# Optimization experiments

Measured on AMD Instinct MI355X. Metric: run time of the kernel, lower is better.

Reference implementation:

```python
import jax, jax.numpy as jnp
import numpy as np

DIM = 1024


def setup_inputs() -> dict:
    key = jax.random.key(0)
    ks = jax.random.split(key, 10)
    B, S, D = 4, 2048, DIM
    std = 1.0 / np.sqrt(D)  # torch Linear default uniform bound
    return {
        "query": jax.random.normal(ks[0], (B, S, D), jnp.float32),
        "key": jax.random.normal(ks[1], (B, S, D), jnp.float32),
        "value": jax.random.normal(ks[2], (B, S, D), jnp.float32),
        "context": jnp.zeros((D,), jnp.float32),
        "Wq": jax.random.uniform(ks[3], (D, D), jnp.float32, -std, std),
        "bq": jax.random.uniform(ks[4], (D,), jnp.float32, -std, std),
        "Wk": jax.random.uniform(ks[5], (D, D), jnp.float32, -std, std),
        "bk": jax.random.uniform(ks[6], (D,), jnp.float32, -std, std),
        "Wv": jax.random.uniform(ks[7], (D, D), jnp.float32, -std, std),
        "bv": jax.random.uniform(ks[8], (D,), jnp.float32, -std, std),
    }


def reference(query, key, value, context, Wq, bq, Wk, bk, Wv, bv):
    scale = query.shape[-1] ** -0.5
    # torch Linear: x @ W.T + b
    q = (query + context) @ Wq.T + bq          # [B,S,D]
    k = (key + context) @ Wk.T + bk            # [B,S,D]
    v = value @ Wv.T + bv                      # [B,S,D]
    scores = jnp.einsum("bqd,bkd->bqk", q, k) * scale  # [B,S,S]
    weights = jax.nn.softmax(scores, axis=-1)
    return jnp.einsum("bqk,bkd->bqd", weights, v)
```

## Files before the change

### kernel.cpp

```cpp
#include <hip/hip_runtime.h>

typedef __attribute__((ext_vector_type(8))) short bf16x8;
typedef __attribute__((ext_vector_type(4))) float floatx4;

constexpr int BATCH = 4;
constexpr int SEQ   = 2048;
constexpr int DIMN  = 1024;
constexpr int M1    = BATCH * SEQ;

__device__ __forceinline__ short f2bf(float f) {
    union { float f; unsigned u; } x; x.f = f;
    unsigned r = x.u + 0x7fffu + ((x.u >> 16) & 1u);
    return (short)(r >> 16);
}
__device__ __forceinline__ float bf2f(short s) {
    union { unsigned u; float f; } x; x.u = ((unsigned)(unsigned short)s) << 16;
    return x.f;
}

__device__ __forceinline__ void async16(const void* g, void* l) {
    __builtin_amdgcn_global_load_lds(
        (const __attribute__((address_space(1))) unsigned int*)g,
        (__attribute__((address_space(3))) unsigned int*)l, 16, 0, 0);
}

#define WAITVM(N) asm volatile("s_waitcnt vmcnt(" #N ")" ::: "memory")
#define MEMFENCE  asm volatile("" ::: "memory")
#define BAR()     __builtin_amdgcn_s_barrier()
#define PRIO(x)   __builtin_amdgcn_s_setprio(x)

template<bool OUT_BF16, int WM>
__device__ __forceinline__ void gemm_core(
    const short* __restrict__ Ab, int lda,
    const short* __restrict__ Bb, int ldb,
    void* __restrict__ Cb, int ldc,
    const float* __restrict__ bias, int K, float scale,
    int m0, int n0)
{
    constexpr int ACH  = WM / 2;
    constexpr int ABY  = WM * 4096;
    constexpr int BUFB = ABY + 32768;
    __shared__ alignas(16) char smem[2][BUFB];
    char* lds = &smem[0][0];

    const int t    = threadIdx.x;
    const int lane = t & 63;
    const int wave = t >> 6;
    const int wr   = wave >> 2;
    const int wc   = wave & 3;
    const int lr   = lane & 15;
    const int lq   = lane >> 4;

    const int srow = t >> 3;
    const int scol = (((t & 7) * 16) ^ (((t >> 3) & 7) << 4)) >> 1;
    const short* pa = Ab + (size_t)(m0 + srow) * lda + scol;
    const short* pb = Bb + (size_t)(n0 + srow) * ldb + scol;
    const size_t rsa = (size_t)64 * lda;
    const size_t rsb = (size_t)64 * ldb;
    const int ldst = t * 16;

    const int roA0 = (wr * (WM * 16) + lr) * 128;
    const int roB0 = ABY + (wc * 64 + lr) * 128;
    const int cp0  = (lq << 4) ^ ((lane & 7) << 4);

    floatx4 acc[WM][4];
    #pragma unroll
    for (int m = 0; m < WM; ++m)
        #pragma unroll
        for (int n = 0; n < 4; ++n) acc[m][n] = (floatx4)(0.f);

    auto stA = [&](int dstb) {
        #pragma unroll
        for (int c = 0; c < ACH; ++c)
            async16(pa + (size_t)c * rsa, lds + dstb + c * 8192 + ldst);
        pa += 64;
    };
    auto stB01 = [&](int dstb) {
        async16(pb,       lds + dstb + ABY +        ldst);
        async16(pb + rsb, lds + dstb + ABY + 8192 + ldst);
    };
    auto stB23 = [&](int dstb) {
        async16(pb + 2 * rsb, lds + dstb + ABY + 16384 + ldst);
        async16(pb + 3 * rsb, lds + dstb + ABY + 24576 + ldst);
        pb += 64;
    };

    const int NT = K >> 6;

    stA(0); stB01(0); stB23(0); stA(BUFB);
    if constexpr (WM == 8) WAITVM(4); else WAITVM(2);
    BAR();

    for (int tt = 0; tt < NT; tt += 2) {
        #pragma unroll
        for (int half = 0; half < 2; ++half) {
            const int bufb = half ? BUFB : 0;
            const int tc   = tt + half;
            const char* rb = lds + bufb;

            if constexpr (WM == 8) {
                bf16x8 af[8], bq_[4];
                #pragma unroll
                for (int m = 0; m < 8; ++m)
                    af[m] = *(const bf16x8*)(rb + roA0 + m * 2048 + cp0);
                bq_[0] = *(const bf16x8*)(rb + roB0 +        cp0);
                bq_[1] = *(const bf16x8*)(rb + roB0 + 2048 + cp0);
                if (tc + 1 < NT) stB01(bufb ^ BUFB);
                BAR(); MEMFENCE;
                PRIO(1);
                #pragma unroll
                for (int m = 0; m < 8; ++m) {
                    acc[m][0] = __builtin_amdgcn_mfma_f32_16x16x32_bf16(af[m], bq_[0], acc[m][0], 0, 0, 0);
                    acc[m][1] = __builtin_amdgcn_mfma_f32_16x16x32_bf16(af[m], bq_[1], acc[m][1], 0, 0, 0);
                }
                PRIO(0);
                MEMFENCE; BAR();
                bq_[2] = *(const bf16x8*)(rb + roB0 + 2 * 2048 + cp0);
                bq_[3] = *(const bf16x8*)(rb + roB0 + 3 * 2048 + cp0);
                if (tc + 1 < NT) stB23(bufb ^ BUFB);
                BAR(); MEMFENCE;
                PRIO(1);
                #pragma unroll
                for (int m = 0; m < 8; ++m) {
                    acc[m][2] = __builtin_amdgcn_mfma_f32_16x16x32_bf16(af[m], bq_[2], acc[m][2], 0, 0, 0);
                    acc[m][3] = __builtin_amdgcn_mfma_f32_16x16x32_bf16(af[m], bq_[3], acc[m][3], 0, 0, 0);
                }
                PRIO(0);
                MEMFENCE; BAR();
                #pragma unroll
                for (int m = 0; m < 8; ++m)
                    af[m] = *(const bf16x8*)(rb + roA0 + m * 2048 + (cp0 ^ 64));
                bq_[0] = *(const bf16x8*)(rb + roB0 +        (cp0 ^ 64));
                bq_[1] = *(const bf16x8*)(rb + roB0 + 2048 + (cp0 ^ 64));
                BAR(); MEMFENCE;
                PRIO(1);
                #pragma unroll
                for (int m = 0; m < 8; ++m) {
                    acc[m][0] = __builtin_amdgcn_mfma_f32_16x16x32_bf16(af[m], bq_[0], acc[m][0], 0, 0, 0);
                    acc[m][1] = __builtin_amdgcn_mfma_f32_16x16x32_bf16(af[m], bq_[1], acc[m][1], 0, 0, 0);
                }
                PRIO(0);
                MEMFENCE; BAR();
                bq_[2] = *(const bf16x8*)(rb + roB0 + 2 * 2048 + (cp0 ^ 64));
                bq_[3] = *(const bf16x8*)(rb + roB0 + 3 * 2048 + (cp0 ^ 64));
                if (tc + 2 < NT) stA(bufb);
                BAR(); MEMFENCE;
                PRIO(1);
                #pragma unroll
                for (int m = 0; m < 8; ++m) {
                    acc[m][2] = __builtin_amdgcn_mfma_f32_16x16x32_bf16(af[m], bq_[2], acc[m][2], 0, 0, 0);
                    acc[m][3] = __builtin_amdgcn_mfma_f32_16x16x32_bf16(af[m], bq_[3], acc[m][3], 0, 0, 0);
                }
                PRIO(0);
                MEMFENCE;
                if (tc + 2 < NT)      { WAITVM(4); }
                else if (tc + 1 < NT) { WAITVM(0); }
                BAR();
            } else {
                bf16x8 af[4][2], bq_[2][2];
                #pragma unroll
                for (int m = 0; m < 4; ++m) {
                    af[m][0] = *(const bf16x8*)(rb + roA0 + m * 2048 + cp0);
                    af[m][1] = *(const bf16x8*)(rb + roA0 + m * 2048 + (cp0 ^ 64));
                }
                #pragma unroll
                for (int n = 0; n < 2; ++n) {
                    bq_[n][0] = *(const bf16x8*)(rb + roB0 + n * 2048 + cp0);
                    bq_[n][1] = *(const bf16x8*)(rb + roB0 + n * 2048 + (cp0 ^ 64));
                }
                if (tc + 1 < NT) { stB01(bufb ^ BUFB); stB23(bufb ^ BUFB); }
                BAR(); MEMFENCE;
                PRIO(1);
                #pragma unroll
                for (int m = 0; m < 4; ++m)
                    #pragma unroll
                    for (int n = 0; n < 2; ++n) {
                        acc[m][n] = __builtin_amdgcn_mfma_f32_16x16x32_bf16(af[m][0], bq_[n][0], acc[m][n], 0, 0, 0);
                        acc[m][n] = __builtin_amdgcn_mfma_f32_16x16x32_bf16(af[m][1], bq_[n][1], acc[m][n], 0, 0, 0);
                    }
                PRIO(0);
                MEMFENCE; BAR();
                #pragma unroll
                for (int n = 0; n < 2; ++n) {
                    bq_[n][0] = *(const bf16x8*)(rb + roB0 + (n + 2) * 2048 + cp0);
                    bq_[n][1] = *(const bf16x8*)(rb + roB0 + (n + 2) * 2048 + (cp0 ^ 64));
                }
                if (tc + 2 < NT) stA(bufb);
                BAR(); MEMFENCE;
                PRIO(1);
                #pragma unroll
                for (int m = 0; m < 4; ++m)
                    #pragma unroll
                    for (int n = 0; n < 2; ++n) {
                        acc[m][n + 2] = __builtin_amdgcn_mfma_f32_16x16x32_bf16(af[m][0], bq_[n][0], acc[m][n + 2], 0, 0, 0);
                        acc[m][n + 2] = __builtin_amdgcn_mfma_f32_16x16x32_bf16(af[m][1], bq_[n][1], acc[m][n + 2], 0, 0, 0);
                    }
                PRIO(0);
                MEMFENCE;
                if (tc + 2 < NT)      { WAITVM(2); }
                else if (tc + 1 < NT) { WAITVM(0); }
                BAR();
            }
        }
    }

    #pragma unroll
    for (int n = 0; n < 4; ++n) {
        const int gn = n0 + wc * 64 + n * 16 + lr;
        const float bv = bias ? bias[gn] : 0.f;
        #pragma unroll
        for (int m = 0; m < WM; ++m) {
            #pragma unroll
            for (int r = 0; r < 4; ++r) {
                const int gm = m0 + wr * (WM * 16) + m * 16 + lq * 4 + r;
                const float v = acc[m][n][r] * scale + bv;
                if (OUT_BF16) ((short*)Cb)[(size_t)gm * ldc + gn] = f2bf(v);
                else          ((float*)Cb)[(size_t)gm * ldc + gn] = v;
            }
        }
    }
}

__global__ __launch_bounds__(512, 2)
void proj_qkv(const short* __restrict__ xq, const short* __restrict__ xk,
              const short* __restrict__ xv,
              const short* __restrict__ Wq_, const short* __restrict__ Wk_,
              const short* __restrict__ Wv_,
              const float* __restrict__ bq_, const float* __restrict__ bk_,
              const float* __restrict__ bv_,
              short* __restrict__ q, short* __restrict__ k, short* __restrict__ vp)
{
    const int b   = blockIdx.x;
    const int xcd = b & 7;
    const int i   = b >> 3;
    const int z   = i >> 5;
    const int r   = i & 31;
    const int mm  = r >> 2;
    const int nn  = r & 3;
    const short* X = (z == 0) ? xq : (z == 1) ? xk : xv;
    const short* W = (z == 0) ? Wq_ : (z == 1) ? Wk_ : Wv_;
    const float* bb = (z == 0) ? bq_ : (z == 1) ? bk_ : bv_;
    short* O = (z == 0) ? q : (z == 1) ? k : vp;
    gemm_core<true, 4>(X, DIMN, W, DIMN, (void*)O, DIMN, bb, DIMN, 1.f,
                       (xcd * 8 + mm) * 128, nn * 256);
}

__global__ __launch_bounds__(512, 2)
void gemm_scores(const short* __restrict__ q, const short* __restrict__ k,
                 short* __restrict__ S, float scale)
{
    const int b   = blockIdx.x;
    const int xcd = b & 7;
    const int i   = b >> 3;
    const int bz  = xcd >> 1;
    const int mh  = xcd & 1;
    const int mm  = i >> 3;
    const int nn  = i & 7;
    gemm_core<true, 8>(q + (size_t)bz * SEQ * DIMN, DIMN,
                       k + (size_t)bz * SEQ * DIMN, DIMN,
                       (void*)(S + (size_t)bz * SEQ * SEQ), SEQ,
                       nullptr, DIMN, scale,
                       (mh * 4 + mm) * 256, nn * 256);
}

__global__ __launch_bounds__(512, 2)
void gemm_pv(const short* __restrict__ P, const short* __restrict__ vt,
             float* __restrict__ O)
{
    const int b   = blockIdx.x;
    const int xcd = b & 7;
    const int i   = b >> 3;
    const int bz  = xcd >> 1;
    const int mh  = xcd & 1;
    const int mm  = i >> 2;
    const int nn  = i & 3;
    gemm_core<false, 4>(P  + (size_t)bz * SEQ * SEQ,  SEQ,
                        vt + (size_t)bz * DIMN * SEQ, SEQ,
                        (void*)(O + (size_t)bz * SEQ * DIMN), DIMN,
                        nullptr, SEQ, 1.f,
                        (mh * 8 + mm) * 128, nn * 256);
}

__global__ __launch_bounds__(256)
void cvt_tri(const float* __restrict__ in0, short* __restrict__ out0,
             const float* __restrict__ in1, short* __restrict__ out1,
             const float* __restrict__ in2, short* __restrict__ out2, int n8)
{
    const int z = blockIdx.z;
    const float* in = (z == 0) ? in0 : (z == 1) ? in1 : in2;
    short* out      = (z == 0) ? out0 : (z == 1) ? out1 : out2;
    const int i = blockIdx.x * 256 + threadIdx.x;
    if (i >= n8) return;
    const float4 a0 = ((const float4*)in)[(size_t)i * 2];
    const float4 a1 = ((const float4*)in)[(size_t)i * 2 + 1];
    const float v[8] = {a0.x, a0.y, a0.z, a0.w, a1.x, a1.y, a1.z, a1.w};
    bf16x8 o;
    #pragma unroll
    for (int j = 0; j < 8; ++j) o[j] = f2bf(v[j]);
    *(bf16x8*)(out + (size_t)i * 8) = o;
}

__global__ __launch_bounds__(256)
void bias3(const float* __restrict__ Wq, const float* __restrict__ Wk,
           const float* __restrict__ Wv,
           const float* __restrict__ bq, const float* __restrict__ bk,
           const float* __restrict__ bv,
           const float* __restrict__ ctx,
           float* __restrict__ oq, float* __restrict__ ok, float* __restrict__ ov)
{
    const int z = blockIdx.y;
    const float* W = (z == 0) ? Wq : (z == 1) ? Wk : Wv;
    const float* b = (z == 0) ? bq : (z == 1) ? bk : bv;
    float*       o = (z == 0) ? oq : (z == 1) ? ok : ov;
    const int n    = blockIdx.x * 4 + (threadIdx.x >> 6);
    const int lane = threadIdx.x & 63;
    float s = 0.f;
    if (z < 2) {
        const float* row = W + (size_t)n * DIMN;
        for (int k = lane * 4; k < DIMN; k += 256) {
            const float4 x = *(const float4*)(row + k);
            const float4 c = *(const float4*)(ctx + k);
            s += x.x * c.x + x.y * c.y + x.z * c.z + x.w * c.w;
        }
        #pragma unroll
        for (int off = 32; off > 0; off >>= 1) s += __shfl_xor(s, off);
    }
    if (lane == 0) o[n] = b[n] + s;
}

__global__ __launch_bounds__(256)
void transpose_v(const short* __restrict__ in, short* __restrict__ out)
{
    __shared__ short t[64][68];
    const int b  = blockIdx.z;
    const int d0 = blockIdx.x * 64;
    const int s0 = blockIdx.y * 64;
    const int r  = threadIdx.x >> 3;
    const int c  = (threadIdx.x & 7) * 8;
    #pragma unroll
    for (int h = 0; h < 2; ++h) {
        const int s = r + h * 32;
        bf16x8 v = *(const bf16x8*)(in + ((size_t)b * SEQ + s0 + s) * DIMN + d0 + c);
        #pragma unroll
        for (int j = 0; j < 8; ++j) t[c + j][s] = v[j];
    }
    __syncthreads();
    #pragma unroll
    for (int h = 0; h < 2; ++h) {
        const int d = r + h * 32;
        bf16x8 v;
        #pragma unroll
        for (int j = 0; j < 8; ++j) v[j] = t[d][c + j];
        *(bf16x8*)(out + ((size_t)b * DIMN + d0 + d) * SEQ + s0 + c) = v;
    }
}

__global__ __launch_bounds__(256)
void softmax_kernel(short* __restrict__ P)
{
    const int bid = blockIdx.x;
    const int xcd = bid & 7;
    const int i   = bid >> 3;
    const int row = (xcd >> 1) * SEQ + (xcd & 1) * 1024 + i;
    short* p = P + (size_t)row * SEQ;
    const int t    = threadIdx.x;
    const int lane = t & 63;
    const int wave = t >> 6;
    __shared__ float red[8];

    bf16x8 raw = *(const bf16x8*)(p + t * 8);
    float v[8];
    float mx = -1e30f;
    #pragma unroll
    for (int j = 0; j < 8; ++j) { v[j] = bf2f(raw[j]); mx = fmaxf(mx, v[j]); }
    #pragma unroll
    for (int off = 32; off > 0; off >>= 1) mx = fmaxf(mx, __shfl_xor(mx, off));
    if (lane == 0) red[wave] = mx;
    __syncthreads();
    mx = fmaxf(fmaxf(red[0], red[1]), fmaxf(red[2], red[3]));

    float e[8], s = 0.f;
    #pragma unroll
    for (int j = 0; j < 8; ++j) { e[j] = __expf(v[j] - mx); s += e[j]; }
    #pragma unroll
    for (int off = 32; off > 0; off >>= 1) s += __shfl_xor(s, off);
    if (lane == 0) red[4 + wave] = s;
    __syncthreads();
    s = red[4] + red[5] + red[6] + red[7];
    const float inv = 1.f / s;

    bf16x8 o;
    #pragma unroll
    for (int j = 0; j < 8; ++j) o[j] = f2bf(e[j] * inv);
    *(bf16x8*)(p + t * 8) = o;
}

extern "C" void kernel_launch(void* const* d_in, const int* in_sizes, int n_in,
                              void* d_out, int out_size, void* d_ws, size_t ws_size,
                              hipStream_t stream)
{
    const float* query = (const float*)d_in[0];
    const float* key_  = (const float*)d_in[1];
    const float* value = (const float*)d_in[2];
    const float* ctx   = (const float*)d_in[3];
    const float* Wq    = (const float*)d_in[4];
    const float* bq    = (const float*)d_in[5];
    const float* Wk    = (const float*)d_in[6];
    const float* bk    = (const float*)d_in[7];
    const float* Wv    = (const float*)d_in[8];
    const float* bv    = (const float*)d_in[9];

    char* ws = (char*)d_ws;
    char* od = (char*)d_out;
    const size_t MB = 1ull << 20;
    short* xq   = (short*)(ws);
    short* xk   = (short*)(ws + 16 * MB);
    short* q_b  = (short*)(ws + 32 * MB);
    short* k_b  = (short*)(ws + 48 * MB);
    short* Wq_b = (short*)(ws + 64 * MB);
    short* Wk_b = (short*)(ws + 66 * MB);
    short* Wv_b = (short*)(ws + 68 * MB);
    float* bq_e = (float*)(ws + 70 * MB);
    float* bk_e = (float*)(ws + 70 * MB + 4096);
    float* bv_e = (float*)(ws + 70 * MB + 8192);
    short* S_b  = (short*)(ws);
    short* v_t  = (short*)(ws + 64 * MB);
    short* xv   = (short*)(od);
    short* vp   = (short*)(od + 16 * MB);

    dim3 blk(256);
    dim3 blk512(512);
    const int W8 = DIMN * DIMN / 8;
    const int X8 = M1 * DIMN / 8;

    cvt_tri<<<dim3(W8 / 256, 1, 3), blk, 0, stream>>>(Wq, Wq_b, Wk, Wk_b, Wv, Wv_b, W8);
    bias3<<<dim3(DIMN / 4, 3), blk, 0, stream>>>(Wq, Wk, Wv, bq, bk, bv, ctx,
                                                 bq_e, bk_e, bv_e);
    cvt_tri<<<dim3(X8 / 256, 1, 3), blk, 0, stream>>>(query, xq, key_, xk, value, xv, X8);

    proj_qkv<<<dim3(768), blk512, 0, stream>>>(xq, xk, xv, Wq_b, Wk_b, Wv_b,
                                               bq_e, bk_e, bv_e, q_b, k_b, vp);
    transpose_v<<<dim3(DIMN / 64, SEQ / 64, BATCH), blk, 0, stream>>>(vp, v_t);

    const float scale = 1.0f / 32.0f;
    gemm_scores<<<dim3(256), blk512, 0, stream>>>(q_b, k_b, S_b, scale);

    softmax_kernel<<<dim3(M1), blk, 0, stream>>>(S_b);

    gemm_pv<<<dim3(256), blk512, 0, stream>>>(S_b, v_t, (float*)d_out);
}
```

Baseline: 304.3 us.

## Restructure GEMM pipelines: triple-buffer 128-row tiles, finer-grained staging for 256-row tiles

Splits the shared GEMM core into two specialized variants. The 128-row variant used by the projection and PV GEMMs now triple-buffers LDS, prefetching two K-tiles ahead to hide global load latency. The 256-row variant used for scores processes one K-tile per iteration, split into four MFMA phases, with its async loads spread across those phases instead of being tied to a two-tile unrolled loop. The triple buffer takes 144KB of LDS per block, which may limit occupancy to one block per CU despite the launch bound of two.

```diff
diff --git a/kernel.cpp b/kernel.cpp
--- a/kernel.cpp
+++ b/kernel.cpp
@@ -29,19 +29,18 @@
 #define BAR()     __builtin_amdgcn_s_barrier()
 #define PRIO(x)   __builtin_amdgcn_s_setprio(x)
 
-template<bool OUT_BF16, int WM>
-__device__ __forceinline__ void gemm_core(
+template<bool OUT_BF16>
+__device__ __forceinline__ void gemm256(
     const short* __restrict__ Ab, int lda,
     const short* __restrict__ Bb, int ldb,
     void* __restrict__ Cb, int ldc,
     const float* __restrict__ bias, int K, float scale,
     int m0, int n0)
 {
-    constexpr int ACH  = WM / 2;
-    constexpr int ABY  = WM * 4096;
-    constexpr int BUFB = ABY + 32768;
-    __shared__ alignas(16) char smem[2][BUFB];
-    char* lds = &smem[0][0];
+    constexpr int ABY  = 32768;
+    constexpr int BUFB = 65536;
+    __shared__ alignas(16) char smem[2 * BUFB];
+    char* lds = smem;
 
     const int t    = threadIdx.x;
     const int lane = t & 63;
@@ -51,157 +50,112 @@
     const int lr   = lane & 15;
     const int lq   = lane >> 4;
 
-    const int srow = t >> 3;
-    const int scol = (((t & 7) * 16) ^ (((t >> 3) & 7) << 4)) >> 1;
-    const short* pa = Ab + (size_t)(m0 + srow) * lda + scol;
-    const short* pb = Bb + (size_t)(n0 + srow) * ldb + scol;
+    const int srow  = t >> 3;
+    const int scol  = (((t & 7) * 16) ^ ((srow & 7) << 4)) >> 1;
+    const short* pa0 = Ab + (size_t)(m0 + srow) * lda + scol;
+    const short* pb0 = Bb + (size_t)(n0 + srow) * ldb + scol;
     const size_t rsa = (size_t)64 * lda;
     const size_t rsb = (size_t)64 * ldb;
     const int ldst = t * 16;
 
-    const int roA0 = (wr * (WM * 16) + lr) * 128;
-    const int roB0 = ABY + (wc * 64 + lr) * 128;
-    const int cp0  = (lq << 4) ^ ((lane & 7) << 4);
-
-    floatx4 acc[WM][4];
-    #pragma unroll
-    for (int m = 0; m < WM; ++m)
+    const int roA = (wr * 128 + lr) * 128;
+    const int roB = ABY + (wc * 64 + lr) * 128;
+    const int cs  = (lane & 7) << 4;
+    const int cp0 = (lq << 4) ^ cs;
+    const int cp1 = (64 | (lq << 4)) ^ cs;
+
+    floatx4 acc[8][4];
+    #pragma unroll
+    for (int m = 0; m < 8; ++m)
         #pragma unroll
         for (int n = 0; n < 4; ++n) acc[m][n] = (floatx4)(0.f);
 
-    auto stA = [&](int dstb) {
-        #pragma unroll
-        for (int c = 0; c < ACH; ++c)
-            async16(pa + (size_t)c * rsa, lds + dstb + c * 8192 + ldst);
-        pa += 64;
-    };
-    auto stB01 = [&](int dstb) {
-        async16(pb,       lds + dstb + ABY +        ldst);
-        async16(pb + rsb, lds + dstb + ABY + 8192 + ldst);
-    };
-    auto stB23 = [&](int dstb) {
-        async16(pb + 2 * rsb, lds + dstb + ABY + 16384 + ldst);
-        async16(pb + 3 * rsb, lds + dstb + ABY + 24576 + ldst);
-        pb += 64;
-    };
+    auto stB01 = [&](int d, int kt) { const short* p = pb0 + kt * 64;
+        async16(p,       lds + d + ABY +        ldst);
+        async16(p + rsb, lds + d + ABY + 8192 + ldst); };
+    auto stB23 = [&](int d, int kt) { const short* p = pb0 + kt * 64;
+        async16(p + 2 * rsb, lds + d + ABY + 16384 + ldst);
+        async16(p + 3 * rsb, lds + d + ABY + 24576 + ldst); };
+    auto stA02 = [&](int d, int kt) { const short* p = pa0 + kt * 64;
+        async16(p,           lds + d +         ldst);
+        async16(p + 2 * rsa, lds + d + 16384 + ldst); };
+    auto stA13 = [&](int d, int kt) { const short* p = pa0 + kt * 64;
+        async16(p + rsa,     lds + d +  8192 + ldst);
+        async16(p + 3 * rsa, lds + d + 24576 + ldst); };
 
     const int NT = K >> 6;
 
-    stA(0); stB01(0); stB23(0); stA(BUFB);
-    if constexpr (WM == 8) WAITVM(4); else WAITVM(2);
-    BAR();
-
-    for (int tt = 0; tt < NT; tt += 2) {
-        #pragma unroll
-        for (int half = 0; half < 2; ++half) {
-            const int bufb = half ? BUFB : 0;
-            const int tc   = tt + half;
-            const char* rb = lds + bufb;
-
-            if constexpr (WM == 8) {
-                bf16x8 af[8], bq_[4];
-                #pragma unroll
-                for (int m = 0; m < 8; ++m)
-                    af[m] = *(const bf16x8*)(rb + roA0 + m * 2048 + cp0);
-                bq_[0] = *(const bf16x8*)(rb + roB0 +        cp0);
-                bq_[1] = *(const bf16x8*)(rb + roB0 + 2048 + cp0);
-                if (tc + 1 < NT) stB01(bufb ^ BUFB);
-                BAR(); MEMFENCE;
-                PRIO(1);
-                #pragma unroll
-                for (int m = 0; m < 8; ++m) {
-                    acc[m][0] = __builtin_amdgcn_mfma_f32_16x16x32_bf16(af[m], bq_[0], acc[m][0], 0, 0, 0);
-                    acc[m][1] = __builtin_amdgcn_mfma_f32_16x16x32_bf16(af[m], bq_[1], acc[m][1], 0, 0, 0);
-                }
-                PRIO(0);
-                MEMFENCE; BAR();
-                bq_[2] = *(const bf16x8*)(rb + roB0 + 2 * 2048 + cp0);
-                bq_[3] = *(const bf16x8*)(rb + roB0 + 3 * 2048 + cp0);
-                if (tc + 1 < NT) stB23(bufb ^ BUFB);
-                BAR(); MEMFENCE;
-                PRIO(1);
-                #pragma unroll
-                for (int m = 0; m < 8; ++m) {
-                    acc[m][2] = __builtin_amdgcn_mfma_f32_16x16x32_bf16(af[m], bq_[2], acc[m][2], 0, 0, 0);
-                    acc[m][3] = __builtin_amdgcn_mfma_f32_16x16x32_bf16(af[m], bq_[3], acc[m][3], 0, 0, 0);
-                }
-                PRIO(0);
-                MEMFENCE; BAR();
-                #pragma unroll
-                for (int m = 0; m < 8; ++m)
-                    af[m] = *(const bf16x8*)(rb + roA0 + m * 2048 + (cp0 ^ 64));
-                bq_[0] = *(const bf16x8*)(rb + roB0 +        (cp0 ^ 64));
-                bq_[1] = *(const bf16x8*)(rb + roB0 + 2048 + (cp0 ^ 64));
-                BAR(); MEMFENCE;
-                PRIO(1);
-                #pragma unroll
-                for (int m = 0; m < 8; ++m) {
-                    acc[m][0] = __builtin_amdgcn_mfma_f32_16x16x32_bf16(af[m], bq_[0], acc[m][0], 0, 0, 0);
-                    acc[m][1] = __builtin_amdgcn_mfma_f32_16x16x32_bf16(af[m], bq_[1], acc[m][1], 0, 0, 0);
-                }
-                PRIO(0);
-                MEMFENCE; BAR();
-                bq_[2] = *(const bf16x8*)(rb + roB0 + 2 * 2048 + (cp0 ^ 64));
-                bq_[3] = *(const bf16x8*)(rb + roB0 + 3 * 2048 + (cp0 ^ 64));
-                if (tc + 2 < NT) stA(bufb);
-                BAR(); MEMFENCE;
-                PRIO(1);
-                #pragma unroll
-                for (int m = 0; m < 8; ++m) {
-                    acc[m][2] = __builtin_amdgcn_mfma_f32_16x16x32_bf16(af[m], bq_[2], acc[m][2], 0, 0, 0);
-                    acc[m][3] = __builtin_amdgcn_mfma_f32_16x16x32_bf16(af[m], bq_[3], acc[m][3], 0, 0, 0);
-                }
-                PRIO(0);
-                MEMFENCE;
-                if (tc + 2 < NT)      { WAITVM(4); }
-                else if (tc + 1 < NT) { WAITVM(0); }
-                BAR();
-            } else {
-                bf16x8 af[4][2], bq_[2][2];
-                #pragma unroll
-                for (int m = 0; m < 4; ++m) {
-                    af[m][0] = *(const bf16x8*)(rb + roA0 + m * 2048 + cp0);
-                    af[m][1] = *(const bf16x8*)(rb + roA0 + m * 2048 + (cp0 ^ 64));
-                }
-                #pragma unroll
-                for (int n = 0; n < 2; ++n) {
-                    bq_[n][0] = *(const bf16x8*)(rb + roB0 + n * 2048 + cp0);
-                    bq_[n][1] = *(const bf16x8*)(rb + roB0 + n * 2048 + (cp0 ^ 64));
-                }
-                if (tc + 1 < NT) { stB01(bufb ^ BUFB); stB23(bufb ^ BUFB); }
-                BAR(); MEMFENCE;
-                PRIO(1);
-                #pragma unroll
-                for (int m = 0; m < 4; ++m)
-                    #pragma unroll
-                    for (int n = 0; n < 2; ++n) {
-                        acc[m][n] = __builtin_amdgcn_mfma_f32_16x16x32_bf16(af[m][0], bq_[n][0], acc[m][n], 0, 0, 0);
-                        acc[m][n] = __builtin_amdgcn_mfma_f32_16x16x32_bf16(af[m][1], bq_[n][1], acc[m][n], 0, 0, 0);
-                    }
-                PRIO(0);
-                MEMFENCE; BAR();
-                #pragma unroll
-                for (int n = 0; n < 2; ++n) {
-                    bq_[n][0] = *(const bf16x8*)(rb + roB0 + (n + 2) * 2048 + cp0);
-                    bq_[n][1] = *(const bf16x8*)(rb + roB0 + (n + 2) * 2048 + (cp0 ^ 64));
-                }
-                if (tc + 2 < NT) stA(bufb);
-                BAR(); MEMFENCE;
-                PRIO(1);
-                #pragma unroll
-                for (int m = 0; m < 4; ++m)
-                    #pragma unroll
-                    for (int n = 0; n < 2; ++n) {
-                        acc[m][n + 2] = __builtin_amdgcn_mfma_f32_16x16x32_bf16(af[m][0], bq_[n][0], acc[m][n + 2], 0, 0, 0);
-                        acc[m][n + 2] = __builtin_amdgcn_mfma_f32_16x16x32_bf16(af[m][1], bq_[n][1], acc[m][n + 2], 0, 0, 0);
-                    }
-                PRIO(0);
-                MEMFENCE;
-                if (tc + 2 < NT)      { WAITVM(2); }
-                else if (tc + 1 < NT) { WAITVM(0); }
-                BAR();
-            }
+    stB01(0, 0); stB23(0, 0); stA02(0, 0); stA13(0, 0);
+    if (NT > 1) { stB01(BUFB, 1); WAITVM(2); }
+    else        { WAITVM(0); }
+    BAR(); MEMFENCE;
+
+    int bu = 0;
+    for (int tt = 0; tt < NT; ++tt) {
+        const int ob = bu ^ BUFB;
+        const char* rb = lds + bu;
+        bf16x8 a0[4], a1[4], bf4[4];
+
+        #pragma unroll
+        for (int m = 0; m < 4; ++m) a0[m]  = *(const bf16x8*)(rb + roA + m * 2048 + cp0);
+        #pragma unroll
+        for (int n = 0; n < 4; ++n) bf4[n] = *(const bf16x8*)(rb + roB + n * 2048 + cp0);
+        if (tt + 1 < NT) stB23(ob, tt + 1);
+        BAR(); MEMFENCE;
+        PRIO(1);
+        #pragma unroll
+        for (int m = 0; m < 4; ++m)
+            #pragma unroll
+            for (int n = 0; n < 4; ++n)
+                acc[m][n] = __builtin_amdgcn_mfma_f32_16x16x32_bf16(a0[m], bf4[n], acc[m][n], 0, 0, 0);
+        PRIO(0); MEMFENCE;
+        if (tt + 1 < NT) { WAITVM(4); } else { WAITVM(0); }
+        BAR(); MEMFENCE;
+
+        #pragma unroll
+        for (int m = 0; m < 4; ++m) a1[m] = *(const bf16x8*)(rb + roA + (m + 4) * 2048 + cp0);
+        if (tt + 1 < NT) stA02(ob, tt + 1);
+        BAR(); MEMFENCE;
+        PRIO(1);
+        #pragma unroll
+        for (int m = 0; m < 4; ++m)
+            #pragma unroll
+            for (int n = 0; n < 4; ++n)
+                acc[m + 4][n] = __builtin_amdgcn_mfma_f32_16x16x32_bf16(a1[m], bf4[n], acc[m + 4][n], 0, 0, 0);
+        PRIO(0); MEMFENCE;
+        BAR(); MEMFENCE;
+
+        #pragma unroll
+        for (int m = 0; m < 4; ++m) a0[m]  = *(const bf16x8*)(rb + roA + m * 2048 + cp1);
+        #pragma unroll
+        for (int n = 0; n < 4; ++n) bf4[n] = *(const bf16x8*)(rb + roB + n * 2048 + cp1);
+        if (tt + 1 < NT) stA13(ob, tt + 1);
+        BAR(); MEMFENCE;
+        PRIO(1);
+        #pragma unroll
+        for (int m = 0; m < 4; ++m)
+            #pragma unroll
+            for (int n = 0; n < 4; ++n)
+                acc[m][n] = __builtin_amdgcn_mfma_f32_16x16x32_bf16(a0[m], bf4[n], acc[m][n], 0, 0, 0);
+        PRIO(0); MEMFENCE;
+        BAR(); MEMFENCE;
+
+        #pragma unroll
+        for (int m = 0; m < 4; ++m) a1[m] = *(const bf16x8*)(rb + roA + (m + 4) * 2048 + cp1);
+        if (tt + 2 < NT) stB01(bu, tt + 2);
+        BAR(); MEMFENCE;
+        PRIO(1);
+        #pragma unroll
+        for (int m = 0; m < 4; ++m)
+            #pragma unroll
+            for (int n = 0; n < 4; ++n)
+                acc[m + 4][n] = __builtin_amdgcn_mfma_f32_16x16x32_bf16(a1[m], bf4[n], acc[m + 4][n], 0, 0, 0);
+        PRIO(0); MEMFENCE;
+        if (tt + 1 < NT) {
+            if (tt + 2 < NT) { WAITVM(4); } else { WAITVM(2); }
         }
+        BAR(); MEMFENCE;
+        bu = ob;
     }
 
     #pragma unroll
@@ -209,10 +163,126 @@
         const int gn = n0 + wc * 64 + n * 16 + lr;
         const float bv = bias ? bias[gn] : 0.f;
         #pragma unroll
-        for (int m = 0; m < WM; ++m) {
+        for (int m = 0; m < 8; ++m) {
             #pragma unroll
             for (int r = 0; r < 4; ++r) {
-                const int gm = m0 + wr * (WM * 16) + m * 16 + lq * 4 + r;
+                const int gm = m0 + wr * 128 + m * 16 + lq * 4 + r;
+                const float v = acc[m][n][r] * scale + bv;
+                if (OUT_BF16) ((short*)Cb)[(size_t)gm * ldc + gn] = f2bf(v);
+                else          ((float*)Cb)[(size_t)gm * ldc + gn] = v;
+            }
+        }
+    }
+}
+
+template<bool OUT_BF16>
+__device__ __forceinline__ void gemm128(
+    const short* __restrict__ Ab, int lda,
+    const short* __restrict__ Bb, int ldb,
+    void* __restrict__ Cb, int ldc,
+    const float* __restrict__ bias, int K, float scale,
+    int m0, int n0)
+{
+    constexpr int ABY  = 16384;
+    constexpr int BUFB = ABY + 32768;
+    __shared__ alignas(16) char smem[3 * BUFB];
+    char* lds = smem;
+
+    const int t    = threadIdx.x;
+    const int lane = t & 63;
+    const int wave = t >> 6;
+    const int wr   = wave >> 2;
+    const int wc   = wave & 3;
+    const int lr   = lane & 15;
+    const int lq   = lane >> 4;
+
+    const int srow  = t >> 3;
+    const int scol  = (((t & 7) * 16) ^ ((srow & 7) << 4)) >> 1;
+    const short* pa0 = Ab + (size_t)(m0 + srow) * lda + scol;
+    const short* pb0 = Bb + (size_t)(n0 + srow) * ldb + scol;
+    const size_t rsa = (size_t)64 * lda;
+    const size_t rsb = (size_t)64 * ldb;
+    const int ldst = t * 16;
+
+    const int roA = (wr * 64 + lr) * 128;
+    const int roB = ABY + (wc * 64 + lr) * 128;
+    const int cs  = (lane & 7) << 4;
+    const int cp0 = (lq << 4) ^ cs;
+    const int cp1 = (64 | (lq << 4)) ^ cs;
+
+    floatx4 acc[4][4];
+    #pragma unroll
+    for (int m = 0; m < 4; ++m)
+        #pragma unroll
+        for (int n = 0; n < 4; ++n) acc[m][n] = (floatx4)(0.f);
+
+    auto stA = [&](int d, int kt) { const short* p = pa0 + kt * 64;
+        async16(p,       lds + d +        ldst);
+        async16(p + rsa, lds + d + 8192 + ldst); };
+    auto stB01 = [&](int d, int kt) { const short* p = pb0 + kt * 64;
+        async16(p,       lds + d + ABY +        ldst);
+        async16(p + rsb, lds + d + ABY + 8192 + ldst); };
+    auto stB23 = [&](int d, int kt) { const short* p = pb0 + kt * 64;
+        async16(p + 2 * rsb, lds + d + ABY + 16384 + ldst);
+        async16(p + 3 * rsb, lds + d + ABY + 24576 + ldst); };
+
+    const int NT = K >> 6;
+
+    stA(0, 0); stB01(0, 0); stB23(0, 0);
+    if (NT > 1) { stA(BUFB, 1); stB01(BUFB, 1); stB23(BUFB, 1); WAITVM(6); }
+    else        { WAITVM(0); }
+    BAR(); MEMFENCE;
+
+    int cb = 0;
+    for (int tt = 0; tt < NT; ++tt) {
+        const char* rb = lds + cb;
+        int sb = cb + 2 * BUFB; if (sb >= 3 * BUFB) sb -= 3 * BUFB;
+        bf16x8 a[4], b[4];
+
+        #pragma unroll
+        for (int m = 0; m < 4; ++m) a[m] = *(const bf16x8*)(rb + roA + m * 2048 + cp0);
+        #pragma unroll
+        for (int n = 0; n < 4; ++n) b[n] = *(const bf16x8*)(rb + roB + n * 2048 + cp0);
+        if (tt + 2 < NT) { stA(sb, tt + 2); stB01(sb, tt + 2); }
+        BAR(); MEMFENCE;
+        PRIO(1);
+        #pragma unroll
+        for (int m = 0; m < 4; ++m)
+            #pragma unroll
+            for (int n = 0; n < 4; ++n)
+                acc[m][n] = __builtin_amdgcn_mfma_f32_16x16x32_bf16(a[m], b[n], acc[m][n], 0, 0, 0);
+        PRIO(0); MEMFENCE;
+        BAR(); MEMFENCE;
+
+        #pragma unroll
+        for (int m = 0; m < 4; ++m) a[m] = *(const bf16x8*)(rb + roA + m * 2048 + cp1);
+        #pragma unroll
+        for (int n = 0; n < 4; ++n) b[n] = *(const bf16x8*)(rb + roB + n * 2048 + cp1);
+        if (tt + 2 < NT) stB23(sb, tt + 2);
+        BAR(); MEMFENCE;
+        PRIO(1);
+        #pragma unroll
+        for (int m = 0; m < 4; ++m)
+            #pragma unroll
+            for (int n = 0; n < 4; ++n)
+                acc[m][n] = __builtin_amdgcn_mfma_f32_16x16x32_bf16(a[m], b[n], acc[m][n], 0, 0, 0);
+        PRIO(0); MEMFENCE;
+        if (tt + 1 < NT) {
+            if (tt + 2 < NT) { WAITVM(6); } else { WAITVM(0); }
+        }
+        BAR(); MEMFENCE;
+        cb += BUFB; if (cb >= 3 * BUFB) cb = 0;
+    }
+
+    #pragma unroll
+    for (int n = 0; n < 4; ++n) {
+        const int gn = n0 + wc * 64 + n * 16 + lr;
+        const float bv = bias ? bias[gn] : 0.f;
+        #pragma unroll
+        for (int m = 0; m < 4; ++m) {
+            #pragma unroll
+            for (int r = 0; r < 4; ++r) {
+                const int gm = m0 + wr * 64 + m * 16 + lq * 4 + r;
                 const float v = acc[m][n][r] * scale + bv;
                 if (OUT_BF16) ((short*)Cb)[(size_t)gm * ldc + gn] = f2bf(v);
                 else          ((float*)Cb)[(size_t)gm * ldc + gn] = v;
@@ -241,8 +311,8 @@
     const short* W = (z == 0) ? Wq_ : (z == 1) ? Wk_ : Wv_;
     const float* bb = (z == 0) ? bq_ : (z == 1) ? bk_ : bv_;
     short* O = (z == 0) ? q : (z == 1) ? k : vp;
-    gemm_core<true, 4>(X, DIMN, W, DIMN, (void*)O, DIMN, bb, DIMN, 1.f,
-                       (xcd * 8 + mm) * 128, nn * 256);
+    gemm128<true>(X, DIMN, W, DIMN, (void*)O, DIMN, bb, DIMN, 1.f,
+                  (xcd * 8 + mm) * 128, nn * 256);
 }
 
 __global__ __launch_bounds__(512, 2)
@@ -256,11 +326,11 @@
     const int mh  = xcd & 1;
     const int mm  = i >> 3;
     const int nn  = i & 7;
-    gemm_core<true, 8>(q + (size_t)bz * SEQ * DIMN, DIMN,
-                       k + (size_t)bz * SEQ * DIMN, DIMN,
-                       (void*)(S + (size_t)bz * SEQ * SEQ), SEQ,
-                       nullptr, DIMN, scale,
-                       (mh * 4 + mm) * 256, nn * 256);
+    gemm256<true>(q + (size_t)bz * SEQ * DIMN, DIMN,
+                  k + (size_t)bz * SEQ * DIMN, DIMN,
+                  (void*)(S + (size_t)bz * SEQ * SEQ), SEQ,
+                  nullptr, DIMN, scale,
+                  (mh * 4 + mm) * 256, nn * 256);
 }
 
 __global__ __launch_bounds__(512, 2)
@@ -274,11 +344,11 @@
     const int mh  = xcd & 1;
     const int mm  = i >> 2;
     const int nn  = i & 3;
-    gemm_core<false, 4>(P  + (size_t)bz * SEQ * SEQ,  SEQ,
-                        vt + (size_t)bz * DIMN * SEQ, SEQ,
-                        (void*)(O + (size_t)bz * SEQ * DIMN), DIMN,
-                        nullptr, SEQ, 1.f,
-                        (mh * 8 + mm) * 128, nn * 256);
+    gemm128<false>(P  + (size_t)bz * SEQ * SEQ,  SEQ,
+                   vt + (size_t)bz * DIMN * SEQ, SEQ,
+                   (void*)(O + (size_t)bz * SEQ * DIMN), DIMN,
+                   nullptr, SEQ, 1.f,
+                   (mh * 8 + mm) * 128, nn * 256);
 }
 
 __global__ __launch_bounds__(256)
```

Result: no change. 308.6 us (+1.4%).
